# Kernel optimization log

Hardware: AMD Instinct MI355X
Metric: run time of the kernel (lower is better)

## Reference

```python
import jax, jax.numpy as jnp
import numpy as np

ALPHA = 2.0  # spikingjelly default ATan surrogate alpha
EPS = 1e-5   # BatchNorm eps

@jax.custom_vjp
def heaviside_atan(x):
    return (x >= 0.0).astype(x.dtype)

def _ha_fwd(x):
    return heaviside_atan(x), x

def _ha_bwd(x, g):
    return (g * ALPHA / (2.0 * (1.0 + (jnp.pi / 2.0 * ALPHA * x) ** 2)),)

heaviside_atan.defvjp(_ha_fwd, _ha_bwd)

def lif(x_seq, tau=2.0, v_th=1.0):
    # MultiStepLIFNode, v_reset=0 (hard reset), detach_reset=True
    def step(v, x):
        v = v + (x - v) / tau
        s = heaviside_atan(v - v_th)
        v = v * (1.0 - jax.lax.stop_gradient(s))
        return v, s
    _, spikes = jax.lax.scan(step, jnp.zeros_like(x_seq[0]), x_seq)
    return spikes

def conv_bn(y, Wt, g, b):
    # 1x1 conv (no bias) + BatchNorm2d in training mode over flattened (T*B, H, W)
    y = jnp.einsum('tbchw,oc->tbohw', y, Wt)
    m = y.mean(axis=(0, 1, 3, 4), keepdims=True)
    v = y.var(axis=(0, 1, 3, 4), keepdims=True)
    C = Wt.shape[0]
    return (y - m) / jnp.sqrt(v + EPS) * g.reshape(1, 1, C, 1, 1) + b.reshape(1, 1, C, 1, 1)

def setup_inputs() -> dict:
    key = jax.random.key(0)
    ks = jax.random.split(key, 5)
    T, B, C, H, W = 4, 64, 384, 14, 14
    x = jax.random.normal(ks[0], (T, B, C, H, W), dtype=jnp.float32)
    Wq = jax.random.normal(ks[1], (C, C), dtype=jnp.float32) * 0.02
    Wk = jax.random.normal(ks[2], (C, C), dtype=jnp.float32) * 0.02
    Wv = jax.random.normal(ks[3], (C, C), dtype=jnp.float32) * 0.02
    Wp = jax.random.normal(ks[4], (C, C), dtype=jnp.float32) * 0.02
    ones = jnp.ones((C,), jnp.float32)
    zeros = jnp.zeros((C,), jnp.float32)
    return {"x": x, "Wq": Wq, "Wk": Wk, "Wv": Wv, "Wp": Wp,
            "gq": ones, "bq": zeros, "gk": ones, "bk": zeros,
            "gv": ones, "bv": zeros, "gp": ones, "bp": zeros}

def reference(x, Wq, Wk, Wv, Wp, gq, bq, gk, bk, gv, bv, gp, bp):
    T, B, C, H, W = x.shape
    nh = 8
    dh = C // nh
    N = H * W

    xs = lif(x)  # pre_lif

    def heads(y):  # [T,B,C,H,W] -> [T,B,h,N,dh]
        y = y.reshape(T, B, C, N).transpose(0, 1, 3, 2)
        return y.reshape(T, B, N, nh, dh).transpose(0, 1, 3, 2, 4)

    q = heads(lif(conv_bn(xs, Wq, gq, bq)))
    k = heads(lif(conv_bn(xs, Wk, gk, bk)))
    v = heads(lif(conv_bn(xs, Wv, gv, bv)))

    attn = jnp.einsum('tbhnd,tbhmd->tbhnm', q, k)      # no softmax
    o = jnp.einsum('tbhnm,tbhmd->tbhnd', attn, v) * 0.125
    o = o.transpose(0, 1, 2, 4, 3).reshape(T, B, C, N).reshape(T, B, C, H, W)
    o = lif(o, v_th=0.5)                                # attn_lif
    return conv_bn(o, Wp, gp, bp)                       # proj (no lif)
```

## Files before the change

kernel.cpp:

```cpp
#include <hip/hip_runtime.h>
#include <hip/hip_bf16.h>
#include <stdint.h>

#define T_  4
#define B_  64
#define C_  384
#define N_  196
#define NH  8
#define DH  48
#define TB_ (T_*B_)
#define R_  (T_*B_*N_)
#define NW  12
#define CBLK 12544
#define SA_  64

typedef float f32x2 __attribute__((ext_vector_type(2)));

__global__ void transpose_w4(const float* __restrict__ s0, const float* __restrict__ s1,
                             const float* __restrict__ s2, const float* __restrict__ s3,
                             float* __restrict__ dst){
    int m = blockIdx.y;
    const float* src = (m==0)?s0:(m==1)?s1:(m==2)?s2:s3;
    int idx = blockIdx.x*256 + threadIdx.x;
    if (idx >= C_*C_) return;
    int o = idx % C_, c = idx / C_;
    dst[(size_t)m*C_*C_ + idx] = src[o*C_ + c];
}

__global__ __launch_bounds__(256) void pre_lif(const float* __restrict__ x,
                                               uint32_t* __restrict__ maskXS){
    int b = blockIdx.x / NW;
    int w = blockIdx.x % NW;
    int n = threadIdx.x;
    if (n >= N_) return;
    float v[32];
#pragma unroll
    for (int j=0;j<32;j++) v[j] = 0.f;
#pragma unroll
    for (int t=0;t<T_;t++){
        uint32_t word = 0;
#pragma unroll
        for (int j=0;j<32;j++){
            int c = w*32 + j;
            float xv = x[((size_t)(t*B_+b)*C_ + c)*N_ + n];
            v[j] = v[j] + (xv - v[j])*0.5f;
            if (v[j] >= 1.0f){ word |= (1u<<j); v[j] = 0.f; }
        }
        maskXS[((size_t)(t*B_+b)*N_ + n)*NW + w] = word;
    }
}

__global__ __launch_bounds__(256) void conv_stats(const uint32_t* __restrict__ mask,
                                                  const float* __restrict__ WT,
                                                  float* __restrict__ Y,
                                                  float* __restrict__ p1,
                                                  float* __restrict__ p2){
    __shared__ float red[4][C_];
    int tid = threadIdx.x, wave = tid>>6, lane = tid&63;
    int pix = blockIdx.x*4 + wave;
    int ob  = 6*lane;
    const uint4* m4 = (const uint4*)(mask + (size_t)pix*NW);
    uint4 ma = m4[0], mb = m4[1], mc = m4[2];
    uint32_t mwv[12] = {ma.x,ma.y,ma.z,ma.w, mb.x,mb.y,mb.z,mb.w, mc.x,mc.y,mc.z,mc.w};
    f32x2 y0={0.f,0.f}, y1={0.f,0.f}, y2={0.f,0.f};
    f32x2 z0={0.f,0.f}, z1={0.f,0.f}, z2={0.f,0.f};
#pragma unroll
    for (int w=0; w<NW; w++){
        uint32_t bits = mwv[w];
        while (bits){
            int c0 = (w<<5) + __builtin_ctz(bits); bits &= bits-1;
            const f32x2* col0 = (const f32x2*)(WT + (size_t)c0*C_ + ob);
            if (bits){
                int c1 = (w<<5) + __builtin_ctz(bits); bits &= bits-1;
                const f32x2* col1 = (const f32x2*)(WT + (size_t)c1*C_ + ob);
                f32x2 a0=col0[0],a1=col0[1],a2=col0[2];
                f32x2 b0=col1[0],b1=col1[1],b2=col1[2];
                y0+=a0; y1+=a1; y2+=a2;
                z0+=b0; z1+=b1; z2+=b2;
            } else {
                y0+=col0[0]; y1+=col0[1]; y2+=col0[2];
            }
        }
    }
    y0+=z0; y1+=z1; y2+=z2;
    f32x2* yo = (f32x2*)(Y + (size_t)pix*C_ + ob);
    yo[0]=y0; yo[1]=y1; yo[2]=y2;
    *(f32x2*)&red[wave][ob  ] = y0;
    *(f32x2*)&red[wave][ob+2] = y1;
    *(f32x2*)&red[wave][ob+4] = y2;
    __syncthreads();
    for (int i=tid; i<C_; i+=256){
        float v0=red[0][i], v1=red[1][i], v2=red[2][i], v3=red[3][i];
        p1[(size_t)blockIdx.x*C_ + i] = (v0+v1)+(v2+v3);
        p2[(size_t)blockIdx.x*C_ + i] = (v0*v0+v1*v1)+(v2*v2+v3*v3);
    }
}

__global__ __launch_bounds__(384) void statsA(const float* __restrict__ p1,
                                              const float* __restrict__ p2,
                                              float* __restrict__ q1,
                                              float* __restrict__ q2){
    int o = threadIdx.x;
    int blk = blockIdx.x;
    const int ROWS = CBLK / SA_;
    size_t base = (size_t)blk*ROWS*C_ + o;
    float s1=0.f, s2=0.f;
#pragma unroll 4
    for (int r=0;r<ROWS;r++){
        s1 += p1[base + (size_t)r*C_];
        s2 += p2[base + (size_t)r*C_];
    }
    q1[blk*C_ + o] = s1;
    q2[blk*C_ + o] = s2;
}

__global__ __launch_bounds__(384) void statsB(const float* __restrict__ q1,
                                              const float* __restrict__ q2,
                                              const float* __restrict__ g,
                                              const float* __restrict__ bta,
                                              float* __restrict__ scale,
                                              float* __restrict__ shift){
    int o = threadIdx.x;
    float s1=0.f, s2=0.f;
#pragma unroll
    for (int b=0;b<SA_;b++){ s1 += q1[b*C_+o]; s2 += q2[b*C_+o]; }
    float m   = s1 / (float)R_;
    float var = s2 / (float)R_ - m*m;
    float sc  = g[o] / sqrtf(var + 1e-5f);
    scale[o] = sc;
    shift[o] = bta[o] - m*sc;
}

__global__ __launch_bounds__(384) void lif_pack(const float* __restrict__ Y,
                                                const float* __restrict__ scale,
                                                const float* __restrict__ shift,
                                                uint32_t* __restrict__ maskOut){
    int pix0 = blockIdx.x;
    int o = threadIdx.x;
    float sc = scale[o];
    float sh = shift[o];
    int w = o >> 6, lane = o & 63;
    float v = 0.f;
#pragma unroll
    for (int t=0;t<T_;t++){
        size_t pix = (size_t)t*B_*N_ + pix0;
        float y = Y[pix*C_ + o]*sc + sh;
        v = v + (y - v)*0.5f;
        int s = (v >= 1.0f);
        unsigned long long bal = __ballot(s);
        if (s) v = 0.f;
        if (lane == 0){
            maskOut[pix*NW + 2*w    ] = (uint32_t)bal;
            maskOut[pix*NW + 2*w + 1] = (uint32_t)(bal >> 32);
        }
    }
}

__global__ __launch_bounds__(256) void attention_lif(const uint32_t* __restrict__ mq,
                                                     const uint32_t* __restrict__ mk,
                                                     const uint32_t* __restrict__ mv,
                                                     uint16_t* __restrict__ mo){
    __shared__ unsigned long long kT[DH][4];
    __shared__ unsigned long long vT[DH][4];
    __shared__ uint32_t Cp[DH*25];

    int h = blockIdx.x & 7;
    int b = blockIdx.x >> 3;
    int tid = threadIdx.x, wv = tid>>6, lane = tid&63;
    int sw  = (h*DH) >> 5;
    int shf = (h*DH) & 31;

    float vm[DH];
#pragma unroll
    for (int d=0;d<DH;d++) vm[d] = 0.f;

    for (int t=0;t<T_;t++){
        int tb = t*B_ + b;
        unsigned long long q = 0, kk = 0, vvv = 0;
        if (tid < N_){
            const uint32_t* pq = mq + ((size_t)tb*N_ + tid)*NW + sw;
            const uint32_t* pk = mk + ((size_t)tb*N_ + tid)*NW + sw;
            const uint32_t* pv = mv + ((size_t)tb*N_ + tid)*NW + sw;
            unsigned long long lo, hi;
            lo = pq[0]; hi = pq[1];
            q   = (shf ? ((lo>>16) | (hi<<16)) : (lo | (hi<<32))) & 0xFFFFFFFFFFFFULL;
            lo = pk[0]; hi = pk[1];
            kk  = (shf ? ((lo>>16) | (hi<<16)) : (lo | (hi<<32))) & 0xFFFFFFFFFFFFULL;
            lo = pv[0]; hi = pv[1];
            vvv = (shf ? ((lo>>16) | (hi<<16)) : (lo | (hi<<32))) & 0xFFFFFFFFFFFFULL;
        }
#pragma unroll 1
        for (int d=0; d<DH; d++){
            unsigned long long bk_ = __ballot((int)((kk >>d)&1ull));
            unsigned long long bv_ = __ballot((int)((vvv>>d)&1ull));
            if (lane == 0){ kT[d][wv] = bk_; vT[d][wv] = bv_; }
        }
        __syncthreads();

        if (tid < 240){
            int j  = tid / 5;
            int dg = tid % 5;
            int d0 = dg*10;
            int d1 = (dg==4) ? 48 : d0+10;
            unsigned long long ka=kT[j][0], kb=kT[j][1], kc=kT[j][2], kd=kT[j][3];
            for (int d=d0; d<d1; d+=2){
                uint32_t c0 = (uint32_t)(__popcll(ka&vT[d][0]) + __popcll(kb&vT[d][1])
                            + __popcll(kc&vT[d][2]) + __popcll(kd&vT[d][3]));
                uint32_t c1 = (uint32_t)(__popcll(ka&vT[d+1][0]) + __popcll(kb&vT[d+1][1])
                            + __popcll(kc&vT[d+1][2]) + __popcll(kd&vT[d+1][3]));
                Cp[j*25 + (d>>1)] = c0 | (c1<<16);
            }
        }
        __syncthreads();

        if (tid < N_){
            uint32_t acc[24];
#pragma unroll
            for (int p=0;p<24;p++) acc[p] = 0u;
            unsigned long long qb = q;
            while (qb){
                int j = __builtin_ctzll(qb); qb &= qb-1;
                const uint32_t* row = &Cp[j*25];
#pragma unroll
                for (int p=0;p<24;p++) acc[p] += row[p];
            }
            unsigned long long sp = 0;
#pragma unroll
            for (int d=0; d<DH; d++){
                uint32_t a = (d&1) ? (acc[d>>1]>>16) : (acc[d>>1]&0xFFFFu);
                float o = 0.125f*(float)a;
                vm[d] = vm[d] + (o - vm[d])*0.5f;
                if (vm[d] >= 0.5f){ sp |= (1ull<<d); vm[d] = 0.f; }
            }
            size_t rec = ((size_t)tb*N_ + tid)*24 + 3*h;
            mo[rec]   = (uint16_t)(sp);
            mo[rec+1] = (uint16_t)(sp >> 16);
            mo[rec+2] = (uint16_t)(sp >> 32);
        }
        __syncthreads();
    }
}

__global__ __launch_bounds__(256) void final_norm(const float* __restrict__ Yp,
                                                  const float* __restrict__ scale,
                                                  const float* __restrict__ shift,
                                                  float* __restrict__ out){
    __shared__ float tile[98][65];
    int bid = blockIdx.x;
    int tb   = bid / 12;
    int r    = bid % 12;
    int c0   = (r>>1)*64;
    int n0   = (r&1)*98;
    int lane = threadIdx.x & 63, w = threadIdx.x >> 6;
    for (int n = w; n < 98; n += 4)
        tile[n][lane] = Yp[((size_t)tb*N_ + n0 + n)*C_ + c0 + lane];
    __syncthreads();
    for (int l = w; l < 64; l += 4){
        int c = c0 + l;
        float sc = scale[c], sh = shift[c];
        float* ob = out + ((size_t)tb*C_ + c)*N_ + n0;
        ob[lane] = tile[lane][l]*sc + sh;
        if (lane < 34) ob[64+lane] = tile[64+lane][l]*sc + sh;
    }
}

extern "C" void kernel_launch(void* const* d_in, const int* in_sizes, int n_in,
                              void* d_out, int out_size, void* d_ws, size_t ws_size,
                              hipStream_t stream) {
    const float* x  = (const float*)d_in[0];
    const float* Wq = (const float*)d_in[1];
    const float* Wk = (const float*)d_in[2];
    const float* Wv = (const float*)d_in[3];
    const float* Wp = (const float*)d_in[4];
    const float* gq = (const float*)d_in[5];
    const float* bq = (const float*)d_in[6];
    const float* gk = (const float*)d_in[7];
    const float* bk = (const float*)d_in[8];
    const float* gv = (const float*)d_in[9];
    const float* bv = (const float*)d_in[10];
    const float* gp = (const float*)d_in[11];
    const float* bp = (const float*)d_in[12];

    char* w = (char*)d_ws;
    size_t off = 0;
    float* Ybuf = (float*)(w + off);  off += (size_t)R_*C_*4;
    uint32_t* maskXS = (uint32_t*)(w + off); off += (size_t)R_*NW*4;
    uint32_t* maskQ  = (uint32_t*)(w + off); off += (size_t)R_*NW*4;
    uint32_t* maskK  = (uint32_t*)(w + off); off += (size_t)R_*NW*4;
    uint32_t* maskV  = (uint32_t*)(w + off); off += (size_t)R_*NW*4;
    float* WTall = (float*)(w + off); off += (size_t)4*C_*C_*4;
    float* q1 = (float*)(w + off); off += (size_t)SA_*C_*4;
    float* q2 = (float*)(w + off); off += (size_t)SA_*C_*4;
    float* scaleB = (float*)(w + off); off += C_*4;
    float* shiftB = (float*)(w + off); off += C_*4;
    uint32_t* maskOL = maskXS;

    float* p1 = (float*)d_out;
    float* p2 = ((float*)d_out) + (size_t)CBLK*C_;

    transpose_w4<<<dim3((C_*C_+255)/256, 4),256,0,stream>>>(Wq, Wk, Wv, Wp, WTall);

    pre_lif<<<B_*NW,256,0,stream>>>(x, maskXS);

    const float* Gs[3] = {gq, gk, gv};
    const float* Bs[3] = {bq, bk, bv};
    uint32_t* Ms[3] = {maskQ, maskK, maskV};
    for (int i=0;i<3;i++){
        conv_stats<<<CBLK,256,0,stream>>>(maskXS, WTall + (size_t)i*C_*C_, Ybuf, p1, p2);
        statsA<<<SA_,384,0,stream>>>(p1, p2, q1, q2);
        statsB<<<1,384,0,stream>>>(q1, q2, Gs[i], Bs[i], scaleB, shiftB);
        lif_pack<<<B_*N_,384,0,stream>>>(Ybuf, scaleB, shiftB, Ms[i]);
    }

    attention_lif<<<B_*NH,256,0,stream>>>(maskQ, maskK, maskV, (uint16_t*)maskOL);

    conv_stats<<<CBLK,256,0,stream>>>(maskOL, WTall + (size_t)3*C_*C_, Ybuf, p1, p2);
    statsA<<<SA_,384,0,stream>>>(p1, p2, q1, q2);
    statsB<<<1,384,0,stream>>>(q1, q2, gp, bp, scaleB, shiftB);

    final_norm<<<TB_*12,256,0,stream>>>(Ybuf, scaleB, shiftB, (float*)d_out);
}
```

Measured before the change: 429.5 us.

## Recompute sparse spike convolutions instead of materializing the fp32 conv output

```diff
diff --git a/kernel.cpp b/kernel.cpp
--- a/kernel.cpp
+++ b/kernel.cpp
@@ -11,7 +11,8 @@
 #define TB_ (T_*B_)
 #define R_  (T_*B_*N_)
 #define NW  12
-#define CBLK 12544
+#define P_  12544
+#define SBLK1 3136
 #define SA_  64
 
 typedef float f32x2 __attribute__((ext_vector_type(2)));
@@ -50,49 +51,55 @@
     }
 }
 
-__global__ __launch_bounds__(256) void conv_stats(const uint32_t* __restrict__ mask,
-                                                  const float* __restrict__ WT,
-                                                  float* __restrict__ Y,
-                                                  float* __restrict__ p1,
-                                                  float* __restrict__ p2){
-    __shared__ float red[4][C_];
+__global__ __launch_bounds__(256) void conv_statsO(const uint32_t* __restrict__ mask,
+                                                   const float* __restrict__ WT,
+                                                   float* __restrict__ p1,
+                                                   float* __restrict__ p2){
+    __shared__ float red1[4][C_];
+    __shared__ float red2[4][C_];
     int tid = threadIdx.x, wave = tid>>6, lane = tid&63;
-    int pix = blockIdx.x*4 + wave;
-    int ob  = 6*lane;
-    const uint4* m4 = (const uint4*)(mask + (size_t)pix*NW);
-    uint4 ma = m4[0], mb = m4[1], mc = m4[2];
-    uint32_t mwv[12] = {ma.x,ma.y,ma.z,ma.w, mb.x,mb.y,mb.z,mb.w, mc.x,mc.y,mc.z,mc.w};
-    f32x2 y0={0.f,0.f}, y1={0.f,0.f}, y2={0.f,0.f};
-    f32x2 z0={0.f,0.f}, z1={0.f,0.f}, z2={0.f,0.f};
-#pragma unroll
-    for (int w=0; w<NW; w++){
-        uint32_t bits = mwv[w];
-        while (bits){
-            int c0 = (w<<5) + __builtin_ctz(bits); bits &= bits-1;
-            const f32x2* col0 = (const f32x2*)(WT + (size_t)c0*C_ + ob);
-            if (bits){
-                int c1 = (w<<5) + __builtin_ctz(bits); bits &= bits-1;
-                const f32x2* col1 = (const f32x2*)(WT + (size_t)c1*C_ + ob);
-                f32x2 a0=col0[0],a1=col0[1],a2=col0[2];
-                f32x2 b0=col1[0],b1=col1[1],b2=col1[2];
-                y0+=a0; y1+=a1; y2+=a2;
-                z0+=b0; z1+=b1; z2+=b2;
-            } else {
-                y0+=col0[0]; y1+=col0[1]; y2+=col0[2];
-            }
-        }
-    }
-    y0+=z0; y1+=z1; y2+=z2;
-    f32x2* yo = (f32x2*)(Y + (size_t)pix*C_ + ob);
-    yo[0]=y0; yo[1]=y1; yo[2]=y2;
-    *(f32x2*)&red[wave][ob  ] = y0;
-    *(f32x2*)&red[wave][ob+2] = y1;
-    *(f32x2*)&red[wave][ob+4] = y2;
+    int ob = 6*lane;
+    f32x2 s10={0.f,0.f}, s11={0.f,0.f}, s12={0.f,0.f};
+    f32x2 s20={0.f,0.f}, s21={0.f,0.f}, s22={0.f,0.f};
+    for (int p=0;p<4;p++){
+        int pix = (blockIdx.x*4 + wave)*4 + p;
+        const uint4* m4 = (const uint4*)(mask + (size_t)pix*NW);
+        uint4 ma = m4[0], mb = m4[1], mc = m4[2];
+        uint32_t mwv[12] = {ma.x,ma.y,ma.z,ma.w, mb.x,mb.y,mb.z,mb.w, mc.x,mc.y,mc.z,mc.w};
+        f32x2 y0={0.f,0.f}, y1={0.f,0.f}, y2={0.f,0.f};
+        f32x2 z0={0.f,0.f}, z1={0.f,0.f}, z2={0.f,0.f};
+#pragma unroll
+        for (int w=0; w<NW; w++){
+            uint32_t bits = mwv[w];
+            while (bits){
+                int c0 = (w<<5) + __builtin_ctz(bits); bits &= bits-1;
+                const f32x2* col0 = (const f32x2*)(WT + (size_t)c0*C_ + ob);
+                if (bits){
+                    int c1 = (w<<5) + __builtin_ctz(bits); bits &= bits-1;
+                    const f32x2* col1 = (const f32x2*)(WT + (size_t)c1*C_ + ob);
+                    f32x2 a0=col0[0],a1=col0[1],a2=col0[2];
+                    f32x2 b0=col1[0],b1=col1[1],b2=col1[2];
+                    y0+=a0; y1+=a1; y2+=a2;
+                    z0+=b0; z1+=b1; z2+=b2;
+                } else {
+                    y0+=col0[0]; y1+=col0[1]; y2+=col0[2];
+                }
+            }
+        }
+        y0+=z0; y1+=z1; y2+=z2;
+        s10+=y0; s11+=y1; s12+=y2;
+        s20+=y0*y0; s21+=y1*y1; s22+=y2*y2;
+    }
+    *(f32x2*)&red1[wave][ob  ] = s10;
+    *(f32x2*)&red1[wave][ob+2] = s11;
+    *(f32x2*)&red1[wave][ob+4] = s12;
+    *(f32x2*)&red2[wave][ob  ] = s20;
+    *(f32x2*)&red2[wave][ob+2] = s21;
+    *(f32x2*)&red2[wave][ob+4] = s22;
     __syncthreads();
     for (int i=tid; i<C_; i+=256){
-        float v0=red[0][i], v1=red[1][i], v2=red[2][i], v3=red[3][i];
-        p1[(size_t)blockIdx.x*C_ + i] = (v0+v1)+(v2+v3);
-        p2[(size_t)blockIdx.x*C_ + i] = (v0*v0+v1*v1)+(v2*v2+v3*v3);
+        p1[(size_t)blockIdx.x*C_ + i] = (red1[0][i]+red1[1][i])+(red1[2][i]+red1[3][i]);
+        p2[(size_t)blockIdx.x*C_ + i] = (red2[0][i]+red2[1][i])+(red2[2][i]+red2[3][i]);
     }
 }
 
@@ -102,7 +109,7 @@
                                               float* __restrict__ q2){
     int o = threadIdx.x;
     int blk = blockIdx.x;
-    const int ROWS = CBLK / SA_;
+    const int ROWS = SBLK1 / SA_;
     size_t base = (size_t)blk*ROWS*C_ + o;
     float s1=0.f, s2=0.f;
 #pragma unroll 4
@@ -131,27 +138,60 @@
     shift[o] = bta[o] - m*sc;
 }
 
-__global__ __launch_bounds__(384) void lif_pack(const float* __restrict__ Y,
+__global__ __launch_bounds__(256) void conv_lif(const uint32_t* __restrict__ mask,
+                                                const float* __restrict__ WT,
                                                 const float* __restrict__ scale,
                                                 const float* __restrict__ shift,
-                                                uint32_t* __restrict__ maskOut){
-    int pix0 = blockIdx.x;
-    int o = threadIdx.x;
-    float sc = scale[o];
-    float sh = shift[o];
-    int w = o >> 6, lane = o & 63;
-    float v = 0.f;
-#pragma unroll
+                                                uint32_t* __restrict__ mo){
+    int tid = threadIdx.x, wave = tid>>6, lane = tid&63;
+    int pix0 = blockIdx.x*4 + wave;
+    float sc[6], sh[6], v[6];
+#pragma unroll
+    for (int i=0;i<6;i++){
+        sc[i] = scale[(i<<6)+lane];
+        sh[i] = shift[(i<<6)+lane];
+        v[i]  = 0.f;
+    }
     for (int t=0;t<T_;t++){
-        size_t pix = (size_t)t*B_*N_ + pix0;
-        float y = Y[pix*C_ + o]*sc + sh;
-        v = v + (y - v)*0.5f;
-        int s = (v >= 1.0f);
-        unsigned long long bal = __ballot(s);
-        if (s) v = 0.f;
+        size_t pix = (size_t)t*P_ + pix0;
+        const uint4* m4 = (const uint4*)(mask + pix*NW);
+        uint4 ma = m4[0], mb = m4[1], mc = m4[2];
+        uint32_t mwv[12] = {ma.x,ma.y,ma.z,ma.w, mb.x,mb.y,mb.z,mb.w, mc.x,mc.y,mc.z,mc.w};
+        float y[6] = {0.f,0.f,0.f,0.f,0.f,0.f};
+        float z[6] = {0.f,0.f,0.f,0.f,0.f,0.f};
+#pragma unroll
+        for (int w=0; w<NW; w++){
+            uint32_t bits = mwv[w];
+            while (bits){
+                int c0 = (w<<5) + __builtin_ctz(bits); bits &= bits-1;
+                const float* col0 = WT + (size_t)c0*C_ + lane;
+                if (bits){
+                    int c1 = (w<<5) + __builtin_ctz(bits); bits &= bits-1;
+                    const float* col1 = WT + (size_t)c1*C_ + lane;
+#pragma unroll
+                    for (int i=0;i<6;i++){ y[i]+=col0[i<<6]; z[i]+=col1[i<<6]; }
+                } else {
+#pragma unroll
+                    for (int i=0;i<6;i++) y[i]+=col0[i<<6];
+                }
+            }
+        }
+        uint32_t words[12];
+#pragma unroll
+        for (int i=0;i<6;i++){
+            float val = (y[i]+z[i])*sc[i] + sh[i];
+            v[i] = v[i] + (val - v[i])*0.5f;
+            int s = (v[i] >= 1.0f);
+            unsigned long long bal = __ballot(s);
+            if (s) v[i] = 0.f;
+            words[2*i]   = (uint32_t)bal;
+            words[2*i+1] = (uint32_t)(bal>>32);
+        }
         if (lane == 0){
-            maskOut[pix*NW + 2*w    ] = (uint32_t)bal;
-            maskOut[pix*NW + 2*w + 1] = (uint32_t)(bal >> 32);
+            uint4* o4 = (uint4*)(mo + pix*NW);
+            o4[0] = make_uint4(words[0],words[1],words[2],words[3]);
+            o4[1] = make_uint4(words[4],words[5],words[6],words[7]);
+            o4[2] = make_uint4(words[8],words[9],words[10],words[11]);
         }
     }
 }
@@ -241,26 +281,56 @@
     }
 }
 
-__global__ __launch_bounds__(256) void final_norm(const float* __restrict__ Yp,
-                                                  const float* __restrict__ scale,
-                                                  const float* __restrict__ shift,
-                                                  float* __restrict__ out){
-    __shared__ float tile[98][65];
+__global__ __launch_bounds__(256) void proj_out(const uint32_t* __restrict__ mask,
+                                                const float* __restrict__ WT,
+                                                const float* __restrict__ scale,
+                                                const float* __restrict__ shift,
+                                                float* __restrict__ out){
+    __shared__ float tile[192][98];
     int bid = blockIdx.x;
-    int tb   = bid / 12;
-    int r    = bid % 12;
-    int c0   = (r>>1)*64;
-    int n0   = (r&1)*98;
-    int lane = threadIdx.x & 63, w = threadIdx.x >> 6;
-    for (int n = w; n < 98; n += 4)
-        tile[n][lane] = Yp[((size_t)tb*N_ + n0 + n)*C_ + c0 + lane];
+    int tb = bid>>2, nh = (bid>>1)&1, ch = bid&1;
+    int n0 = nh*98, c0 = ch*192;
+    int tid = threadIdx.x, wave = tid>>6, lane = tid&63;
+    float sc[3], sh[3];
+#pragma unroll
+    for (int i=0;i<3;i++){
+        sc[i] = scale[c0+(i<<6)+lane];
+        sh[i] = shift[c0+(i<<6)+lane];
+    }
+    for (int p=wave; p<98; p+=4){
+        size_t pix = (size_t)tb*N_ + n0 + p;
+        const uint4* m4 = (const uint4*)(mask + pix*NW);
+        uint4 ma = m4[0], mb = m4[1], mc = m4[2];
+        uint32_t mwv[12] = {ma.x,ma.y,ma.z,ma.w, mb.x,mb.y,mb.z,mb.w, mc.x,mc.y,mc.z,mc.w};
+        float y[3] = {0.f,0.f,0.f};
+        float z[3] = {0.f,0.f,0.f};
+#pragma unroll
+        for (int w=0; w<NW; w++){
+            uint32_t bits = mwv[w];
+            while (bits){
+                int cc0 = (w<<5) + __builtin_ctz(bits); bits &= bits-1;
+                const float* col0 = WT + (size_t)cc0*C_ + c0 + lane;
+                if (bits){
+                    int cc1 = (w<<5) + __builtin_ctz(bits); bits &= bits-1;
+                    const float* col1 = WT + (size_t)cc1*C_ + c0 + lane;
+#pragma unroll
+                    for (int i=0;i<3;i++){ y[i]+=col0[i<<6]; z[i]+=col1[i<<6]; }
+                } else {
+#pragma unroll
+                    for (int i=0;i<3;i++) y[i]+=col0[i<<6];
+                }
+            }
+        }
+#pragma unroll
+        for (int i=0;i<3;i++)
+            tile[(i<<6)+lane][p] = (y[i]+z[i])*sc[i] + sh[i];
+    }
     __syncthreads();
-    for (int l = w; l < 64; l += 4){
-        int c = c0 + l;
-        float sc = scale[c], sh = shift[c];
-        float* ob = out + ((size_t)tb*C_ + c)*N_ + n0;
-        ob[lane] = tile[lane][l]*sc + sh;
-        if (lane < 34) ob[64+lane] = tile[64+lane][l]*sc + sh;
+    for (int r=wave; r<192; r+=4){
+        if (lane < 49){
+            f32x2 tv = *(const f32x2*)&tile[r][2*lane];
+            *(f32x2*)(out + ((size_t)tb*C_ + c0 + r)*N_ + n0 + 2*lane) = tv;
+        }
     }
 }
 
@@ -283,21 +353,19 @@
 
     char* w = (char*)d_ws;
     size_t off = 0;
-    float* Ybuf = (float*)(w + off);  off += (size_t)R_*C_*4;
     uint32_t* maskXS = (uint32_t*)(w + off); off += (size_t)R_*NW*4;
     uint32_t* maskQ  = (uint32_t*)(w + off); off += (size_t)R_*NW*4;
     uint32_t* maskK  = (uint32_t*)(w + off); off += (size_t)R_*NW*4;
     uint32_t* maskV  = (uint32_t*)(w + off); off += (size_t)R_*NW*4;
     float* WTall = (float*)(w + off); off += (size_t)4*C_*C_*4;
+    float* p1 = (float*)(w + off); off += (size_t)SBLK1*C_*4;
+    float* p2 = (float*)(w + off); off += (size_t)SBLK1*C_*4;
     float* q1 = (float*)(w + off); off += (size_t)SA_*C_*4;
     float* q2 = (float*)(w + off); off += (size_t)SA_*C_*4;
     float* scaleB = (float*)(w + off); off += C_*4;
     float* shiftB = (float*)(w + off); off += C_*4;
     uint32_t* maskOL = maskXS;
 
-    float* p1 = (float*)d_out;
-    float* p2 = ((float*)d_out) + (size_t)CBLK*C_;
-
     transpose_w4<<<dim3((C_*C_+255)/256, 4),256,0,stream>>>(Wq, Wk, Wv, Wp, WTall);
 
     pre_lif<<<B_*NW,256,0,stream>>>(x, maskXS);
@@ -306,17 +374,19 @@
     const float* Bs[3] = {bq, bk, bv};
     uint32_t* Ms[3] = {maskQ, maskK, maskV};
     for (int i=0;i<3;i++){
-        conv_stats<<<CBLK,256,0,stream>>>(maskXS, WTall + (size_t)i*C_*C_, Ybuf, p1, p2);
+        const float* WT = WTall + (size_t)i*C_*C_;
+        conv_statsO<<<SBLK1,256,0,stream>>>(maskXS, WT, p1, p2);
         statsA<<<SA_,384,0,stream>>>(p1, p2, q1, q2);
         statsB<<<1,384,0,stream>>>(q1, q2, Gs[i], Bs[i], scaleB, shiftB);
-        lif_pack<<<B_*N_,384,0,stream>>>(Ybuf, scaleB, shiftB, Ms[i]);
+        conv_lif<<<P_/4,256,0,stream>>>(maskXS, WT, scaleB, shiftB, Ms[i]);
     }
 
     attention_lif<<<B_*NH,256,0,stream>>>(maskQ, maskK, maskV, (uint16_t*)maskOL);
 
-    conv_stats<<<CBLK,256,0,stream>>>(maskOL, WTall + (size_t)3*C_*C_, Ybuf, p1, p2);
+    const float* WTp = WTall + (size_t)3*C_*C_;
+    conv_statsO<<<SBLK1,256,0,stream>>>(maskOL, WTp, p1, p2);
     statsA<<<SA_,384,0,stream>>>(p1, p2, q1, q2);
     statsB<<<1,384,0,stream>>>(q1, q2, gp, bp, scaleB, shiftB);
 
-    final_norm<<<TB_*12,256,0,stream>>>(Ybuf, scaleB, shiftB, (float*)d_out);
-}
+    proj_out<<<TB_*4,256,0,stream>>>(maskOL, WTp, scaleB, shiftB, (float*)d_out);
+}
```

Result: slower. 445.8 us (+3.8%).
